# Kernel tuning notes

Measured on AMD Instinct MI355X. Metric: run time of the kernel, lower is better.

The kernel has to match this reference:

```python
import jax, jax.numpy as jnp
import numpy as np
import math

EMBED_DIM = 512
NUM_HEADS = 8
HEAD_DIM = EMBED_DIM // NUM_HEADS


def setup_inputs() -> dict:
    key = jax.random.key(0)
    ks = jax.random.split(key, 11)
    s = 1.0 / math.sqrt(EMBED_DIM)
    x = jax.random.normal(ks[0], (8, EMBED_DIM, 32, 32), dtype=jnp.float32)
    Wq = jax.random.uniform(ks[1], (EMBED_DIM, EMBED_DIM), jnp.float32, -s, s)
    bq = jax.random.uniform(ks[2], (EMBED_DIM,), jnp.float32, -s, s)
    Wk = jax.random.uniform(ks[3], (EMBED_DIM, EMBED_DIM), jnp.float32, -s, s)
    bk = jax.random.uniform(ks[4], (EMBED_DIM,), jnp.float32, -s, s)
    Wv = jax.random.uniform(ks[5], (EMBED_DIM, EMBED_DIM), jnp.float32, -s, s)
    bv = jax.random.uniform(ks[6], (EMBED_DIM,), jnp.float32, -s, s)
    Wo = jax.random.uniform(ks[7], (EMBED_DIM, EMBED_DIM), jnp.float32, -s, s)
    bo = jax.random.uniform(ks[8], (EMBED_DIM,), jnp.float32, -s, s)
    gamma = jnp.ones((EMBED_DIM,), jnp.float32)
    beta = jnp.zeros((EMBED_DIM,), jnp.float32)
    return {"x": x, "Wq": Wq, "bq": bq, "Wk": Wk, "bk": bk, "Wv": Wv,
            "bv": bv, "Wo": Wo, "bo": bo, "gamma": gamma, "beta": beta}


def layer_norm(x, gamma, beta, eps=1e-5):
    mu = jnp.mean(x, axis=-1, keepdims=True)
    var = jnp.mean(jnp.square(x - mu), axis=-1, keepdims=True)
    return (x - mu) * jax.lax.rsqrt(var + eps) * gamma + beta


def reference(x, Wq, bq, Wk, bk, Wv, bv, Wo, bo, gamma, beta):
    B, C, H, W = x.shape
    S = H * W
    # [B, S, C]
    x_flat = x.reshape(B, C, S).transpose(0, 2, 1)
    residual = x_flat
    xn = layer_norm(x_flat, gamma, beta)
    # torch Linear: y = x @ W^T + b
    q = (xn @ Wq.T + bq).reshape(B, S, NUM_HEADS, HEAD_DIM)
    k = (xn @ Wk.T + bk).reshape(B, S, NUM_HEADS, HEAD_DIM)
    v = (xn @ Wv.T + bv).reshape(B, S, NUM_HEADS, HEAD_DIM)
    scale = 1.0 / math.sqrt(HEAD_DIM)
    scores = jnp.einsum('bqhd,bkhd->bhqk', q, k) * scale
    attn = jax.nn.softmax(scores, axis=-1)  # dropout is identity in eval
    out = jnp.einsum('bhqk,bkhd->bqhd', attn, v).reshape(B, S, C)
    out = out @ Wo.T + bo + residual
    return out.transpose(0, 2, 1).reshape(B, C, H, W)
```

## Files before the change

kernel.cpp:

```cpp
#include <hip/hip_runtime.h>
#include <hip/hip_bf16.h>

typedef __bf16 bf16_t;
typedef __bf16 bf16x8 __attribute__((ext_vector_type(8)));
typedef float floatx4 __attribute__((ext_vector_type(4)));

#define EMBED 512
#define S_LEN 1024
#define NH 8
#define HD 64
#define LDK 1056
#define LDV 1088

#define MFMA16(a, b, c) __builtin_amdgcn_mfma_f32_16x16x32_bf16(a, b, c, 0, 0, 0)

static __device__ __forceinline__ bf16_t f2bf(float f) {
    unsigned int x = __builtin_bit_cast(unsigned int, f);
    unsigned int lsb = (x >> 16) & 1u;
    x += 0x7fffu + lsb;
    unsigned short u = (unsigned short)(x >> 16);
    return __builtin_bit_cast(bf16_t, u);
}
static __device__ __forceinline__ float bf2f(bf16_t v) {
    unsigned short u = __builtin_bit_cast(unsigned short, v);
    unsigned int x = ((unsigned int)u) << 16;
    return __builtin_bit_cast(float, x);
}
static __device__ __forceinline__ unsigned int pack2(float lo, float hi) {
    return (__builtin_bit_cast(unsigned int, lo) >> 16) |
           (__builtin_bit_cast(unsigned int, hi) & 0xFFFF0000u);
}
static __device__ __forceinline__ unsigned int pack2r(float lo, float hi) {
    unsigned short a = __builtin_bit_cast(unsigned short, f2bf(lo));
    unsigned short b = __builtin_bit_cast(unsigned short, f2bf(hi));
    return (unsigned int)a | ((unsigned int)b << 16);
}

__global__ __launch_bounds__(256) void cvt4_kernel(const float* __restrict__ s0,
                                                   const float* __restrict__ s1,
                                                   const float* __restrict__ s2,
                                                   const float* __restrict__ s3,
                                                   bf16_t* __restrict__ d0,
                                                   bf16_t* __restrict__ d1,
                                                   bf16_t* __restrict__ d2,
                                                   bf16_t* __restrict__ d3) {
    const float* s; bf16_t* d;
    switch (blockIdx.y) {
        case 0:  s = s0; d = d0; break;
        case 1:  s = s1; d = d1; break;
        case 2:  s = s2; d = d2; break;
        default: s = s3; d = d3; break;
    }
    int i = (blockIdx.x * 256 + threadIdx.x) * 8;
#pragma unroll
    for (int j = 0; j < 8; ++j) d[i + j] = f2bf(s[i + j]);
}

__global__ __launch_bounds__(256) void ln_fused_kernel(const float* __restrict__ x,
                                                       const float* __restrict__ gamma,
                                                       const float* __restrict__ beta,
                                                       bf16_t* __restrict__ xn) {
    __shared__ float T[32][521];
    __shared__ float Pm[32][33], Pq[32][33];
    __shared__ float Mu[32], Rs[32];
    int bid = blockIdx.x;
    int b = bid >> 5, s0 = (bid & 31) * 32;
    int t = threadIdx.x;
    int lc = t >> 3;
    int si = (t & 7) * 4;
    const float* xp = x + ((size_t)b * EMBED + lc) * S_LEN + s0 + si;
    float sm[4] = {}, sq[4] = {};
#pragma unroll
    for (int p = 0; p < 16; ++p) {
        int c = lc + p * 32;
        float4 v = *(const float4*)(xp + (size_t)p * 32 * S_LEN);
        int cs = c ^ ((c >> 3) & 0x38);
        T[si + 0][cs] = v.x; T[si + 1][cs] = v.y;
        T[si + 2][cs] = v.z; T[si + 3][cs] = v.w;
        sm[0] += v.x; sq[0] += v.x * v.x;
        sm[1] += v.y; sq[1] += v.y * v.y;
        sm[2] += v.z; sq[2] += v.z * v.z;
        sm[3] += v.w; sq[3] += v.w * v.w;
    }
#pragma unroll
    for (int k = 0; k < 4; ++k) { Pm[si + k][lc] = sm[k]; Pq[si + k][lc] = sq[k]; }
    __syncthreads();
    if (t < 32) {
        float m = 0.f, q = 0.f;
#pragma unroll
        for (int j = 0; j < 32; ++j) { m += Pm[t][j]; q += Pq[t][j]; }
        float mu = m * (1.0f / EMBED);
        float var = q * (1.0f / EMBED) - mu * mu;
        Mu[t] = mu; Rs[t] = rsqrtf(var + 1e-5f);
    }
    __syncthreads();
    int cidx = t & 31;
    int rw = t >> 5;
#pragma unroll
    for (int rg = 0; rg < 4; ++rg) {
        int srl = rg * 8 + rw;
        float mu = Mu[srl], rs = Rs[srl];
        int cb = cidx * 16;
        bf16_t* dst = xn + ((size_t)b * S_LEN + s0 + srl) * EMBED + cb;
#pragma unroll
        for (int h = 0; h < 2; ++h) {
            int c0h = cb + h * 8;
            float4 g0 = *(const float4*)(gamma + c0h);
            float4 g1 = *(const float4*)(gamma + c0h + 4);
            float4 be0 = *(const float4*)(beta + c0h);
            float4 be1 = *(const float4*)(beta + c0h + 4);
            float gv[8] = {g0.x, g0.y, g0.z, g0.w, g1.x, g1.y, g1.z, g1.w};
            float bv[8] = {be0.x, be0.y, be0.z, be0.w, be1.x, be1.y, be1.z, be1.w};
            bf16x8 o;
#pragma unroll
            for (int j = 0; j < 8; ++j) {
                int c = c0h + j;
                int cs = c ^ ((c >> 3) & 0x38);
                o[j] = f2bf((T[srl][cs] - mu) * rs * gv[j] + bv[j]);
            }
            *(bf16x8*)(dst + h * 8) = o;
        }
    }
}

__global__ __launch_bounds__(256) void gemm_kernel(const bf16_t* __restrict__ X,
                                                   const bf16_t* __restrict__ W,
                                                   const float* __restrict__ b0,
                                                   const float* __restrict__ b1,
                                                   const float* __restrict__ b2,
                                                   bf16_t* __restrict__ Y,
                                                   bf16_t* __restrict__ vtb) {
    __shared__ __align__(16) bf16_t Wl[2][128 * 72];
    int t = threadIdx.x;
    int col0 = blockIdx.y * 128, row0 = blockIdx.x * 128;
    int scol = t >> 1, sseg = (t & 1) * 32;
    const bf16_t* wsrc = W + (size_t)(col0 + scol) * EMBED + sseg;
    {
        bf16x8 r0 = *(const bf16x8*)(wsrc);
        bf16x8 r1 = *(const bf16x8*)(wsrc + 8);
        bf16x8 r2 = *(const bf16x8*)(wsrc + 16);
        bf16x8 r3 = *(const bf16x8*)(wsrc + 24);
        bf16_t* d = &Wl[0][scol * 72 + sseg];
        *(bf16x8*)d = r0;        *(bf16x8*)(d + 8) = r1;
        *(bf16x8*)(d + 16) = r2; *(bf16x8*)(d + 24) = r3;
    }
    int lane = t & 63, w = t >> 6, g = lane >> 4, n16 = lane & 15;
    int rw0 = row0 + w * 32;
    const bf16_t* xr0 = X + (size_t)(rw0 + n16) * EMBED + g * 8;
    const bf16_t* xr1 = xr0 + (size_t)16 * EMBED;
    bf16x8 a00 = *(const bf16x8*)(xr0);
    bf16x8 a01 = *(const bf16x8*)(xr0 + 32);
    bf16x8 a10 = *(const bf16x8*)(xr1);
    bf16x8 a11 = *(const bf16x8*)(xr1 + 32);
    __syncthreads();
    floatx4 acc[2][8] = {};
#pragma unroll
    for (int kc = 0; kc < 8; ++kc) {
        bf16x8 p0, p1, p2, p3, na00, na01, na10, na11;
        if (kc < 7) {
            int ko = (kc + 1) * 64;
            p0 = *(const bf16x8*)(wsrc + ko);
            p1 = *(const bf16x8*)(wsrc + ko + 8);
            p2 = *(const bf16x8*)(wsrc + ko + 16);
            p3 = *(const bf16x8*)(wsrc + ko + 24);
            na00 = *(const bf16x8*)(xr0 + ko);
            na01 = *(const bf16x8*)(xr0 + ko + 32);
            na10 = *(const bf16x8*)(xr1 + ko);
            na11 = *(const bf16x8*)(xr1 + ko + 32);
        }
        const bf16_t* wl = &Wl[kc & 1][0];
#pragma unroll
        for (int kk = 0; kk < 2; ++kk) {
            bf16x8 s0 = (kk == 0) ? a00 : a01;
            bf16x8 s1 = (kk == 0) ? a10 : a11;
#pragma unroll
            for (int nt = 0; nt < 8; ++nt) {
                bf16x8 bfr = *(const bf16x8*)(&wl[(nt * 16 + n16) * 72 + kk * 32 + g * 8]);
                acc[0][nt] = MFMA16(s0, bfr, acc[0][nt]);
                acc[1][nt] = MFMA16(s1, bfr, acc[1][nt]);
            }
        }
        if (kc < 7) {
            bf16_t* d = &Wl[(kc + 1) & 1][scol * 72 + sseg];
            *(bf16x8*)d = p0;        *(bf16x8*)(d + 8) = p1;
            *(bf16x8*)(d + 16) = p2; *(bf16x8*)(d + 24) = p3;
            a00 = na00; a01 = na01; a10 = na10; a11 = na11;
        }
        __syncthreads();
    }
    if (col0 < 1024) {
        const float* bp = (col0 < 512) ? b0 : b1;
#pragma unroll
        for (int ar = 0; ar < 2; ++ar)
#pragma unroll
            for (int nt = 0; nt < 8; ++nt) {
                int col = col0 + nt * 16 + n16;
                float bv = bp[col & 511];
#pragma unroll
                for (int r = 0; r < 4; ++r) {
                    int row = rw0 + ar * 16 + g * 4 + r;
                    Y[(size_t)row * LDK + col] = f2bf(acc[ar][nt][r] + bv);
                }
            }
    } else {
        bf16_t* Tl = &Wl[0][0];
#pragma unroll
        for (int ar = 0; ar < 2; ++ar)
#pragma unroll
            for (int nt = 0; nt < 8; ++nt) {
                int chl = nt * 16 + n16;
                float bv = b2[(col0 & 511) + chl];
                uint2 pr;
                pr.x = pack2r(acc[ar][nt][0] + bv, acc[ar][nt][1] + bv);
                pr.y = pack2r(acc[ar][nt][2] + bv, acc[ar][nt][3] + bv);
                *(uint2*)(&Tl[chl * 136 + w * 32 + ar * 16 + g * 4]) = pr;
            }
        __syncthreads();
        int ch = t >> 1, seg = (t & 1) * 64;
        int bb = row0 >> 10, s0 = row0 & 1023;
        bf16_t* dst = vtb + ((size_t)(bb * EMBED + (col0 - 1024) + ch)) * LDV + s0 + seg;
        const bf16_t* srcl = &Tl[ch * 136 + seg];
#pragma unroll
        for (int i = 0; i < 8; ++i)
            *(bf16x8*)(dst + i * 8) = *(const bf16x8*)(srcl + i * 8);
    }
}

__global__ __launch_bounds__(256) void wsgemm_out_kernel(const bf16_t* __restrict__ Wb,
                                                         const bf16_t* __restrict__ act,
                                                         const float* __restrict__ bias,
                                                         const float* __restrict__ xres,
                                                         float* __restrict__ out) {
    __shared__ __align__(16) bf16_t Al[2][64 * 72];
    int b = blockIdx.z, n0 = blockIdx.x * 64, m0 = blockIdx.y * 128;
    int t = threadIdx.x;
    int srow = t >> 2, sseg = (t & 3) * 16;
    const bf16_t* asrc = act + ((size_t)b * S_LEN + n0 + srow) * EMBED + sseg;
    {
        bf16x8 r0 = *(const bf16x8*)(asrc);
        bf16x8 r1 = *(const bf16x8*)(asrc + 8);
        bf16_t* d = &Al[0][srow * 72 + sseg];
        *(bf16x8*)d = r0; *(bf16x8*)(d + 8) = r1;
    }
    int lane = t & 63, w = t >> 6, g = lane >> 4, n16 = lane & 15;
    int mw = m0 + w * 32;
    const bf16_t* wr0 = Wb + (size_t)(mw + n16) * EMBED + g * 8;
    const bf16_t* wr1 = wr0 + (size_t)16 * EMBED;
    bf16x8 a00 = *(const bf16x8*)(wr0);
    bf16x8 a01 = *(const bf16x8*)(wr0 + 32);
    bf16x8 a10 = *(const bf16x8*)(wr1);
    bf16x8 a11 = *(const bf16x8*)(wr1 + 32);
    __syncthreads();
    floatx4 acc[2][4] = {};
#pragma unroll
    for (int kc = 0; kc < 8; ++kc) {
        bf16x8 p0, p1, na00, na01, na10, na11;
        if (kc < 7) {
            int ko = (kc + 1) * 64;
            p0 = *(const bf16x8*)(asrc + ko);
            p1 = *(const bf16x8*)(asrc + ko + 8);
            na00 = *(const bf16x8*)(wr0 + ko);
            na01 = *(const bf16x8*)(wr0 + ko + 32);
            na10 = *(const bf16x8*)(wr1 + ko);
            na11 = *(const bf16x8*)(wr1 + ko + 32);
        }
        const bf16_t* al = &Al[kc & 1][0];
#pragma unroll
        for (int kk = 0; kk < 2; ++kk) {
            bf16x8 s0 = (kk == 0) ? a00 : a01;
            bf16x8 s1 = (kk == 0) ? a10 : a11;
#pragma unroll
            for (int nt = 0; nt < 4; ++nt) {
                bf16x8 bfr = *(const bf16x8*)(&al[(nt * 16 + n16) * 72 + kk * 32 + g * 8]);
                acc[0][nt] = MFMA16(s0, bfr, acc[0][nt]);
                acc[1][nt] = MFMA16(s1, bfr, acc[1][nt]);
            }
        }
        if (kc < 7) {
            bf16_t* d = &Al[(kc + 1) & 1][srow * 72 + sseg];
            *(bf16x8*)d = p0; *(bf16x8*)(d + 8) = p1;
            a00 = na00; a01 = na01; a10 = na10; a11 = na11;
        }
        __syncthreads();
    }
#pragma unroll
    for (int ar = 0; ar < 2; ++ar)
#pragma unroll
        for (int r = 0; r < 4; ++r) {
            int row = mw + ar * 16 + g * 4 + r;
            float bv = bias[row];
#pragma unroll
            for (int nt = 0; nt < 4; ++nt) {
                int col = n0 + nt * 16 + n16;
                size_t oi = ((size_t)b * EMBED + row) * S_LEN + col;
                out[oi] = acc[ar][nt][r] + bv + xres[oi];
            }
        }
}

__global__ __launch_bounds__(256) void attn_kernel(const bf16_t* __restrict__ qk,
                                                   const bf16_t* __restrict__ vt,
                                                   bf16_t* __restrict__ o) {
    __shared__ __align__(16) bf16_t Kt[2][64 * 72];
    __shared__ __align__(16) bf16_t Vl2[2][64 * 72];
    __shared__ __align__(16) unsigned int Pl[4][16 * 68];
    int bid = blockIdx.x;
    int bh = bid & 63, qt = bid >> 6;
    int b = bh >> 3, h = bh & 7;
    int t = threadIdx.x, w = t >> 6, lane = t & 63, g = lane >> 4, n16 = lane & 15;
    size_t baseQK = (size_t)b * S_LEN * LDK;
    size_t baseV  = ((size_t)b * EMBED + h * HD) * LDV;
    int qA = qt * 128 + w * 32 + n16;

    const float QSC = 0.18033688f;
    const bf16_t* qpA = qk + baseQK + (size_t)qA * LDK + h * HD + g * 8;
    const bf16_t* qpB = qpA + (size_t)16 * LDK;
    bf16x8 qa0 = *(const bf16x8*)(qpA);
    bf16x8 qa1 = *(const bf16x8*)(qpA + 32);
    bf16x8 qb0 = *(const bf16x8*)(qpB);
    bf16x8 qb1 = *(const bf16x8*)(qpB + 32);
#pragma unroll
    for (int j = 0; j < 8; ++j) {
        qa0[j] = f2bf(bf2f(qa0[j]) * QSC);
        qa1[j] = f2bf(bf2f(qa1[j]) * QSC);
        qb0[j] = f2bf(bf2f(qb0[j]) * QSC);
        qb1[j] = f2bf(bf2f(qb1[j]) * QSC);
    }
    const bf16_t* kbase = qk + baseQK + 512 + h * HD;
    const bf16_t* vbase = vt + baseV;

    int srow = t >> 2, scol = (t & 3) * 16;
    const bf16_t* ksrc = kbase + (size_t)srow * LDK + scol;
    const bf16_t* vsrc = vbase + (size_t)srow * LDV + scol;
    {
        bf16x8 k0 = *(const bf16x8*)(ksrc);
        bf16x8 k1 = *(const bf16x8*)(ksrc + 8);
        bf16x8 v0 = *(const bf16x8*)(vsrc);
        bf16x8 v1 = *(const bf16x8*)(vsrc + 8);
        bf16_t* kd = &Kt[0][srow * 72 + scol];
        bf16_t* vd = &Vl2[0][srow * 72 + scol];
        *(bf16x8*)kd = k0; *(bf16x8*)(kd + 8) = k1;
        *(bf16x8*)vd = v0; *(bf16x8*)(vd + 8) = v1;
    }

    float lsA[4] = {}, lsB[4] = {};
    floatx4 oaccA[4] = {}, oaccB[4] = {};
    unsigned int* PLw = &Pl[w][0];
    const float NEG12L2E = -17.3123405f;

    for (int it = 0; it < 16; ++it) {
        int cur = it & 1, nxt = cur ^ 1;
        __syncthreads();
        bf16x8 pk0, pk1, pv0, pv1;
        if (it < 15) {
            const bf16_t* kp = ksrc + (size_t)(it + 1) * 64 * LDK;
            pk0 = *(const bf16x8*)(kp);
            pk1 = *(const bf16x8*)(kp + 8);
            const bf16_t* vp = vsrc + (it + 1) * 64;
            pv0 = *(const bf16x8*)(vp);
            pv1 = *(const bf16x8*)(vp + 8);
        }
        const bf16_t* Kl = &Kt[cur][0];
        const bf16_t* Vl = &Vl2[cur][0];
        floatx4 sA[4], sB[4];
#pragma unroll
        for (int kb = 0; kb < 4; ++kb) {
            bf16x8 k0 = *(const bf16x8*)(&Kl[(kb * 16 + n16) * 72 + g * 8]);
            bf16x8 k1 = *(const bf16x8*)(&Kl[(kb * 16 + n16) * 72 + 32 + g * 8]);
            sA[kb] = floatx4{NEG12L2E, NEG12L2E, NEG12L2E, NEG12L2E};
            sA[kb] = MFMA16(k0, qa0, sA[kb]);
            sA[kb] = MFMA16(k1, qa1, sA[kb]);
            sB[kb] = floatx4{NEG12L2E, NEG12L2E, NEG12L2E, NEG12L2E};
            sB[kb] = MFMA16(k0, qb0, sB[kb]);
            sB[kb] = MFMA16(k1, qb1, sB[kb]);
        }
#pragma unroll
        for (int kb = 0; kb < 4; ++kb)
#pragma unroll
            for (int r = 0; r < 4; ++r) {
                float eA = exp2f(sA[kb][r]);
                sA[kb][r] = eA; lsA[kb] += eA;
                float eB = exp2f(sB[kb][r]);
                sB[kb][r] = eB; lsB[kb] += eB;
            }
#pragma unroll
        for (int kb = 0; kb < 4; ++kb) {
            uint2 prA, prB;
            prA.x = pack2(sA[kb][0], sA[kb][1]);
            prA.y = pack2(sA[kb][2], sA[kb][3]);
            *(uint2*)&PLw[n16 * 68 + kb * 8 + g * 2] = prA;
            prB.x = pack2(sB[kb][0], sB[kb][1]);
            prB.y = pack2(sB[kb][2], sB[kb][3]);
            *(uint2*)&PLw[n16 * 68 + 32 + kb * 8 + g * 2] = prB;
        }
        uint4 uA0 = *(const uint4*)&PLw[n16 * 68 + g * 4];
        uint4 uA1 = *(const uint4*)&PLw[n16 * 68 + 16 + g * 4];
        uint4 uB0 = *(const uint4*)&PLw[n16 * 68 + 32 + g * 4];
        uint4 uB1 = *(const uint4*)&PLw[n16 * 68 + 48 + g * 4];
        bf16x8 pfA0 = __builtin_bit_cast(bf16x8, uA0);
        bf16x8 pfA1 = __builtin_bit_cast(bf16x8, uA1);
        bf16x8 pfB0 = __builtin_bit_cast(bf16x8, uB0);
        bf16x8 pfB1 = __builtin_bit_cast(bf16x8, uB1);
        if (it < 15) {
            bf16_t* kd = &Kt[nxt][srow * 72 + scol];
            bf16_t* vd = &Vl2[nxt][srow * 72 + scol];
            *(bf16x8*)kd = pk0; *(bf16x8*)(kd + 8) = pk1;
            *(bf16x8*)vd = pv0; *(bf16x8*)(vd + 8) = pv1;
        }
#pragma unroll
        for (int dt = 0; dt < 4; ++dt) {
            bf16x8 v0 = *(const bf16x8*)(&Vl[(dt * 16 + n16) * 72 + g * 8]);
            bf16x8 v1 = *(const bf16x8*)(&Vl[(dt * 16 + n16) * 72 + 32 + g * 8]);
            oaccA[dt] = MFMA16(v0, pfA0, oaccA[dt]);
            oaccA[dt] = MFMA16(v1, pfA1, oaccA[dt]);
            oaccB[dt] = MFMA16(v0, pfB0, oaccB[dt]);
            oaccB[dt] = MFMA16(v1, pfB1, oaccB[dt]);
        }
    }
    float lA = (lsA[0] + lsA[1]) + (lsA[2] + lsA[3]);
    lA += __shfl_xor(lA, 16);
    lA += __shfl_xor(lA, 32);
    float lB = (lsB[0] + lsB[1]) + (lsB[2] + lsB[3]);
    lB += __shfl_xor(lB, 16);
    lB += __shfl_xor(lB, 32);
    float rlA = 1.0f / lA, rlB = 1.0f / lB;
    size_t orowA = ((size_t)b * S_LEN + qA) * EMBED + h * HD;
    size_t orowB = orowA + (size_t)16 * EMBED;
#pragma unroll
    for (int dt = 0; dt < 4; ++dt) {
        uint2 prA, prB;
        prA.x = pack2(oaccA[dt][0] * rlA, oaccA[dt][1] * rlA);
        prA.y = pack2(oaccA[dt][2] * rlA, oaccA[dt][3] * rlA);
        *(uint2*)(o + orowA + dt * 16 + g * 4) = prA;
        prB.x = pack2(oaccB[dt][0] * rlB, oaccB[dt][1] * rlB);
        prB.y = pack2(oaccB[dt][2] * rlB, oaccB[dt][3] * rlB);
        *(uint2*)(o + orowB + dt * 16 + g * 4) = prB;
    }
}

extern "C" void kernel_launch(void* const* d_in, const int* in_sizes, int n_in,
                              void* d_out, int out_size, void* d_ws, size_t ws_size,
                              hipStream_t stream) {
    const float* x     = (const float*)d_in[0];
    const float* Wq    = (const float*)d_in[1];
    const float* bq    = (const float*)d_in[2];
    const float* Wk    = (const float*)d_in[3];
    const float* bk    = (const float*)d_in[4];
    const float* Wv    = (const float*)d_in[5];
    const float* bv    = (const float*)d_in[6];
    const float* Wo    = (const float*)d_in[7];
    const float* bo    = (const float*)d_in[8];
    const float* gamma = (const float*)d_in[9];
    const float* beta  = (const float*)d_in[10];
    float* out = (float*)d_out;

    char* ws = (char*)d_ws;
    bf16_t* xn    = (bf16_t*)ws;
    bf16_t* qkb   = (bf16_t*)(ws + 8388608);
    bf16_t* wqkv  = (bf16_t*)(ws + 25690112);
    bf16_t* wo    = (bf16_t*)(ws + 27262976);
    bf16_t* ab    = xn;

    bf16_t* vtb = (bf16_t*)d_out;

    cvt4_kernel<<<dim3(128, 4), 256, 0, stream>>>(Wq, Wk, Wv, Wo,
                                                  wqkv, wqkv + 262144,
                                                  wqkv + 524288, wo);
    ln_fused_kernel<<<dim3(256), 256, 0, stream>>>(x, gamma, beta, xn);
    gemm_kernel<<<dim3(64, 12), 256, 0, stream>>>(xn, wqkv, bq, bk, bv, qkb, vtb);
    attn_kernel<<<dim3(512), 256, 0, stream>>>(qkb, vtb, ab);
    wsgemm_out_kernel<<<dim3(16, 4, 8), 256, 0, stream>>>(wo, ab, bo, x, out);
}
```

Measured before the change: 169.9 us.

## Load GEMM weight tiles directly to LDS with XOR swizzle; add MFMA priority hints

The projection GEMM now stages weight tiles with global_load_lds (direct global-to-LDS DMA) instead of loading into registers and then storing to LDS. Each tile uses an unpadded 64-wide layout with an XOR swizzle to avoid bank conflicts. This frees registers and removes the LDS store instructions from the loop. The attention kernel also raises wave priority around its MFMA blocks with s_setprio to favour matrix issue. The risk is that the async LDS writes depend on the existing barriers for correctness, and the priority hints may change nothing.

Result: no change. 170.0 us (+0.0%).

```diff
diff --git a/kernel.cpp b/kernel.cpp
--- a/kernel.cpp
+++ b/kernel.cpp
@@ -34,6 +34,11 @@
     unsigned short a = __builtin_bit_cast(unsigned short, f2bf(lo));
     unsigned short b = __builtin_bit_cast(unsigned short, f2bf(hi));
     return (unsigned int)a | ((unsigned int)b << 16);
+}
+static __device__ __forceinline__ void gload16(const bf16_t* g, bf16_t* l) {
+    __builtin_amdgcn_global_load_lds(
+        (const __attribute__((address_space(1))) unsigned int*)g,
+        (__attribute__((address_space(3))) unsigned int*)l, 16, 0, 0);
 }
 
 __global__ __launch_bounds__(256) void cvt4_kernel(const float* __restrict__ s0,
@@ -130,21 +135,19 @@
                                                    const float* __restrict__ b2,
                                                    bf16_t* __restrict__ Y,
                                                    bf16_t* __restrict__ vtb) {
-    __shared__ __align__(16) bf16_t Wl[2][128 * 72];
+    __shared__ __align__(16) bf16_t Sh[2][128 * 72];
+    bf16_t* Wlin = &Sh[0][0];
     int t = threadIdx.x;
     int col0 = blockIdx.y * 128, row0 = blockIdx.x * 128;
-    int scol = t >> 1, sseg = (t & 1) * 32;
-    const bf16_t* wsrc = W + (size_t)(col0 + scol) * EMBED + sseg;
+    int lane = t & 63, w = t >> 6, g = lane >> 4, n16 = lane & 15;
+    int swzk = (((lane & 7) ^ (lane >> 3)) & 7) * 8;
+    const bf16_t* wg = W + (size_t)(col0 + w * 32 + (lane >> 3)) * EMBED + swzk;
+    bf16_t* ldwave = Wlin + (w * 4) * 512;
     {
-        bf16x8 r0 = *(const bf16x8*)(wsrc);
-        bf16x8 r1 = *(const bf16x8*)(wsrc + 8);
-        bf16x8 r2 = *(const bf16x8*)(wsrc + 16);
-        bf16x8 r3 = *(const bf16x8*)(wsrc + 24);
-        bf16_t* d = &Wl[0][scol * 72 + sseg];
-        *(bf16x8*)d = r0;        *(bf16x8*)(d + 8) = r1;
-        *(bf16x8*)(d + 16) = r2; *(bf16x8*)(d + 24) = r3;
-    }
-    int lane = t & 63, w = t >> 6, g = lane >> 4, n16 = lane & 15;
+#pragma unroll
+        for (int j = 0; j < 4; ++j)
+            gload16(wg + (size_t)j * 8 * EMBED, ldwave + j * 512);
+    }
     int rw0 = row0 + w * 32;
     const bf16_t* xr0 = X + (size_t)(rw0 + n16) * EMBED + g * 8;
     const bf16_t* xr1 = xr0 + (size_t)16 * EMBED;
@@ -154,36 +157,35 @@
     bf16x8 a11 = *(const bf16x8*)(xr1 + 32);
     __syncthreads();
     floatx4 acc[2][8] = {};
+    int cs0 = ((g ^ (n16 & 7))) * 8;
 #pragma unroll
     for (int kc = 0; kc < 8; ++kc) {
-        bf16x8 p0, p1, p2, p3, na00, na01, na10, na11;
+        bf16x8 na00, na01, na10, na11;
         if (kc < 7) {
             int ko = (kc + 1) * 64;
-            p0 = *(const bf16x8*)(wsrc + ko);
-            p1 = *(const bf16x8*)(wsrc + ko + 8);
-            p2 = *(const bf16x8*)(wsrc + ko + 16);
-            p3 = *(const bf16x8*)(wsrc + ko + 24);
+            bf16_t* ld = Wlin + ((kc + 1) & 1) * 8192 + (w * 4) * 512;
+#pragma unroll
+            for (int j = 0; j < 4; ++j)
+                gload16(wg + (size_t)j * 8 * EMBED + ko, ld + j * 512);
             na00 = *(const bf16x8*)(xr0 + ko);
             na01 = *(const bf16x8*)(xr0 + ko + 32);
             na10 = *(const bf16x8*)(xr1 + ko);
             na11 = *(const bf16x8*)(xr1 + ko + 32);
         }
-        const bf16_t* wl = &Wl[kc & 1][0];
+        const bf16_t* wb = Wlin + (kc & 1) * 8192;
 #pragma unroll
         for (int kk = 0; kk < 2; ++kk) {
             bf16x8 s0 = (kk == 0) ? a00 : a01;
             bf16x8 s1 = (kk == 0) ? a10 : a11;
+            int csk = cs0 ^ (kk * 32);
 #pragma unroll
             for (int nt = 0; nt < 8; ++nt) {
-                bf16x8 bfr = *(const bf16x8*)(&wl[(nt * 16 + n16) * 72 + kk * 32 + g * 8]);
+                bf16x8 bfr = *(const bf16x8*)(&wb[(nt * 16 + n16) * 64 + csk]);
                 acc[0][nt] = MFMA16(s0, bfr, acc[0][nt]);
                 acc[1][nt] = MFMA16(s1, bfr, acc[1][nt]);
             }
         }
         if (kc < 7) {
-            bf16_t* d = &Wl[(kc + 1) & 1][scol * 72 + sseg];
-            *(bf16x8*)d = p0;        *(bf16x8*)(d + 8) = p1;
-            *(bf16x8*)(d + 16) = p2; *(bf16x8*)(d + 24) = p3;
             a00 = na00; a01 = na01; a10 = na10; a11 = na11;
         }
         __syncthreads();
@@ -203,7 +205,7 @@
                 }
             }
     } else {
-        bf16_t* Tl = &Wl[0][0];
+        bf16_t* Tl = Wlin;
 #pragma unroll
         for (int ar = 0; ar < 2; ++ar)
 #pragma unroll
@@ -363,6 +365,7 @@
         const bf16_t* Kl = &Kt[cur][0];
         const bf16_t* Vl = &Vl2[cur][0];
         floatx4 sA[4], sB[4];
+        __builtin_amdgcn_s_setprio(1);
 #pragma unroll
         for (int kb = 0; kb < 4; ++kb) {
             bf16x8 k0 = *(const bf16x8*)(&Kl[(kb * 16 + n16) * 72 + g * 8]);
@@ -374,6 +377,7 @@
             sB[kb] = MFMA16(k0, qb0, sB[kb]);
             sB[kb] = MFMA16(k1, qb1, sB[kb]);
         }
+        __builtin_amdgcn_s_setprio(0);
 #pragma unroll
         for (int kb = 0; kb < 4; ++kb)
 #pragma unroll
@@ -407,6 +411,7 @@
             *(bf16x8*)kd = pk0; *(bf16x8*)(kd + 8) = pk1;
             *(bf16x8*)vd = pv0; *(bf16x8*)(vd + 8) = pv1;
         }
+        __builtin_amdgcn_s_setprio(1);
 #pragma unroll
         for (int dt = 0; dt < 4; ++dt) {
             bf16x8 v0 = *(const bf16x8*)(&Vl[(dt * 16 + n16) * 72 + g * 8]);
@@ -416,6 +421,7 @@
             oaccB[dt] = MFMA16(v0, pfB0, oaccB[dt]);
             oaccB[dt] = MFMA16(v1, pfB1, oaccB[dt]);
         }
+        __builtin_amdgcn_s_setprio(0);
     }
     float lA = (lsA[0] + lsA[1]) + (lsA[2] + lsA[3]);
     lA += __shfl_xor(lA, 16);
```
